# Optimization experiments

Measured on AMD Instinct MI355X. Metric: run time of the kernel, lower is better.

The kernel has to match this reference:

```python
import jax, jax.numpy as jnp
import numpy as np

# Dims: batch B, seq L, embed D, router hidden H, num_blocks NB, top_k K
B, L, D, H, NB, K = 8, 4096, 1024, 64, 16, 2
TEMP = 2.0          # current_temperature buffer (init 2.0), clamp(min=0.1) inert
LN_EPS = 1e-5


def setup_inputs() -> dict:
    key = jax.random.key(0)
    k_x, k_w1, k_w2 = jax.random.split(key, 3)
    return {
        "x": jax.random.normal(k_x, (B, L, D), dtype=jnp.float32),
        "ln_gamma": jnp.ones((D,), dtype=jnp.float32),
        "ln_beta": jnp.zeros((D,), dtype=jnp.float32),
        "W1": jax.random.normal(k_w1, (D, H), dtype=jnp.float32) / np.sqrt(D).astype(np.float32),
        "W2": jax.random.normal(k_w2, (H, NB), dtype=jnp.float32) / np.sqrt(H).astype(np.float32),
    }


def reference(x, ln_gamma, ln_beta, W1, W2):
    # gate: LayerNorm -> Linear(no bias) -> GELU(exact) -> Linear(no bias)
    mu = jnp.mean(x, axis=-1, keepdims=True)
    var = jnp.mean(jnp.square(x - mu), axis=-1, keepdims=True)
    xn = (x - mu) * jax.lax.rsqrt(var + LN_EPS) * ln_gamma + ln_beta
    h = jax.nn.gelu(xn @ W1, approximate=False)          # (B, L, H)
    logits = (h @ W2) / TEMP                              # (B, L, NB)

    probs = jax.nn.softmax(logits, axis=-1)               # (B, L, NB)
    top_probs, indices = jax.lax.top_k(probs, K)          # (B, L, K) each
    weights = top_probs / (jnp.sum(top_probs, axis=-1, keepdims=True) + 1e-8)

    # load-balancing aux loss: f = fraction of assignments per block (detached),
    # P = mean router prob per block
    counts = jnp.zeros((NB,), dtype=probs.dtype).at[indices.reshape(-1)].add(1.0)
    f = jax.lax.stop_gradient(counts) / (B * L * K + 1e-8)
    P = jnp.mean(probs, axis=(0, 1))                      # (NB,)
    aux_loss = NB * jnp.sum(f * P)

    return probs, indices, aux_loss, weights
```

## Files before the change

kernel.cpp:

```cpp
#include <hip/hip_runtime.h>
#include <math.h>

typedef __attribute__((ext_vector_type(8))) short short8;
typedef __attribute__((ext_vector_type(4))) float f32x4;

#define NTOK 32768
#define DDIM 1024
#define HDIM 64
#define NB 16
#define LN_EPS 1e-5f

#define IDX_OFF ((size_t)NTOK * NB)
#define AUX_OFF (IDX_OFF + (size_t)NTOK * 2)
#define WT_OFF  (AUX_OFF + 1)

#define CS_F   64
#define BP_F   4352
#define PART_F 102656

__device__ __forceinline__ short8 as_s8(uint4 u) {
    union { uint4 u; short8 s; } x; x.u = u; return x.s;
}

__device__ __forceinline__ f32x4 ntload4(const float* p) {
    return __builtin_nontemporal_load((const f32x4*)p);
}

__global__ void pack_kernel(const float* __restrict__ W1,
                            const float* __restrict__ gamma,
                            const float* __restrict__ beta,
                            float* __restrict__ ws) {
    __shared__ float sg[4][64];
    __shared__ float sb[4][64];
    const int s = blockIdx.x;
    const int t = threadIdx.x;

    {
        const int j = t & 63, p = t >> 6;
        float ag = 0.f, ab = 0.f;
        for (int kk = 0; kk < 8; ++kk) {
            const int k = s * 32 + p * 8 + kk;
            const float w = W1[k * HDIM + j];
            ag += gamma[k] * w;
            ab += beta[k] * w;
        }
        sg[p][j] = ag;
        sb[p][j] = ab;
    }

    {
        unsigned int* bp = (unsigned int*)(ws + BP_F);
        const int n = t >> 6;
        const int l = t & 63;
        const int q = l >> 4, c = l & 15;
        const int col = n * 16 + c;
        unsigned int uh[8], um[8], ul[8];
#pragma unroll
        for (int j = 0; j < 8; ++j) {
            const int k = s * 32 + q * 8 + j;
            const float w = gamma[k] * W1[k * HDIM + col];
            const unsigned int hb = __float_as_uint(w) & 0xFFFF0000u;
            const float r = w - __uint_as_float(hb);
            const unsigned int mb = __float_as_uint(r) & 0xFFFF0000u;
            const float r2 = r - __uint_as_float(mb);
            const unsigned int lb = __float_as_uint(r2) & 0xFFFF0000u;
            uh[j] = hb >> 16; um[j] = mb >> 16; ul[j] = lb >> 16;
        }
        const int base = ((s * 4 + n) * 64 + l) * 4;
#pragma unroll
        for (int d = 0; d < 4; ++d) {
            bp[base + d]         = uh[2 * d] | (uh[2 * d + 1] << 16);
            bp[32768 + base + d] = um[2 * d] | (um[2 * d + 1] << 16);
            bp[65536 + base + d] = ul[2 * d] | (ul[2 * d + 1] << 16);
        }
    }
    __syncthreads();
    if (t < 64) {
        atomicAdd(&ws[CS_F + t],      sg[0][t] + sg[1][t] + sg[2][t] + sg[3][t]);
        atomicAdd(&ws[CS_F + 64 + t], sb[0][t] + sb[1][t] + sb[2][t] + sb[3][t]);
    }
}

__device__ __forceinline__ void split8(const f32x4 a0, const f32x4 a1,
                                       short8& AH, short8& AM, short8& AL,
                                       float& s1, float& s2) {
    const float v[8] = {a0.x, a0.y, a0.z, a0.w, a1.x, a1.y, a1.z, a1.w};
    unsigned int ph[4], pm[4], pl[4];
#pragma unroll
    for (int d = 0; d < 4; ++d) {
        const float v0 = v[2 * d], v1 = v[2 * d + 1];
        const unsigned int h0 = __float_as_uint(v0) & 0xFFFF0000u;
        const unsigned int h1 = __float_as_uint(v1) & 0xFFFF0000u;
        const float r0 = v0 - __uint_as_float(h0);
        const float r1 = v1 - __uint_as_float(h1);
        const unsigned int m0 = __float_as_uint(r0) & 0xFFFF0000u;
        const unsigned int m1 = __float_as_uint(r1) & 0xFFFF0000u;
        const float q0 = r0 - __uint_as_float(m0);
        const float q1 = r1 - __uint_as_float(m1);
        ph[d] = (h0 >> 16) | h1;
        pm[d] = (m0 >> 16) | m1;
        pl[d] = (__float_as_uint(q0) >> 16) | (__float_as_uint(q1) & 0xFFFF0000u);
        s1 += v0 + v1;
        s2 = fmaf(v0, v0, fmaf(v1, v1, s2));
    }
    AH = as_s8(make_uint4(ph[0], ph[1], ph[2], ph[3]));
    AM = as_s8(make_uint4(pm[0], pm[1], pm[2], pm[3]));
    AL = as_s8(make_uint4(pl[0], pl[1], pl[2], pl[3]));
}

#define MFMA6(ACC, AH, AM, AL, BH, BM, BL)                                        \
    ACC = __builtin_amdgcn_mfma_f32_16x16x32_bf16(AH, as_s8(BH), ACC, 0, 0, 0);   \
    ACC = __builtin_amdgcn_mfma_f32_16x16x32_bf16(AH, as_s8(BM), ACC, 0, 0, 0);   \
    ACC = __builtin_amdgcn_mfma_f32_16x16x32_bf16(AM, as_s8(BH), ACC, 0, 0, 0);   \
    ACC = __builtin_amdgcn_mfma_f32_16x16x32_bf16(AH, as_s8(BL), ACC, 0, 0, 0);   \
    ACC = __builtin_amdgcn_mfma_f32_16x16x32_bf16(AM, as_s8(BM), ACC, 0, 0, 0);   \
    ACC = __builtin_amdgcn_mfma_f32_16x16x32_bf16(AL, as_s8(BH), ACC, 0, 0, 0);

#define STEP(S, CUR, NXT, DOSTAGE)                                               \
    {                                                                            \
        const int off = (((S) + 2) & 31) * 32;                                   \
        const f32x4 p00 = ntload4(xr0 + off), p01 = ntload4(xr0 + off + 4);      \
        const f32x4 p10 = ntload4(xr1 + off), p11 = ntload4(xr1 + off + 4);      \
        uint4 st0, st1, st2;                                                     \
        if (DOSTAGE) {                                                           \
            const unsigned int* sp = bp + ((S) + 1) * 1024 + t * 4;              \
            st0 = *(const uint4*)(sp);                                           \
            st1 = *(const uint4*)(sp + 32768);                                   \
            st2 = *(const uint4*)(sp + 65536);                                   \
        }                                                                        \
        short8 AH0, AM0, AL0, AH1, AM1, AL1;                                     \
        split8(a00, a01, AH0, AM0, AL0, s1a, s2a);                               \
        split8(a10, a11, AH1, AM1, AL1, s1b, s2b);                               \
        _Pragma("unroll")                                                        \
        for (int n = 0; n < 4; ++n) {                                            \
            const uint4 bh = *(const uint4*)((CUR) + n * 256 + lane * 4);        \
            const uint4 bm = *(const uint4*)((CUR) + 1024 + n * 256 + lane * 4); \
            const uint4 bl = *(const uint4*)((CUR) + 2048 + n * 256 + lane * 4); \
            MFMA6(acc0[n], AH0, AM0, AL0, bh, bm, bl);                           \
            MFMA6(acc1[n], AH1, AM1, AL1, bh, bm, bl);                           \
        }                                                                        \
        a00 = b00; a01 = b01; a10 = b10; a11 = b11;                              \
        b00 = p00; b01 = p01; b10 = p10; b11 = p11;                              \
        if (DOSTAGE) {                                                           \
            *(uint4*)((NXT) + t * 4)        = st0;                               \
            *(uint4*)((NXT) + 1024 + t * 4) = st1;                               \
            *(uint4*)((NXT) + 2048 + t * 4) = st2;                               \
        }                                                                        \
        __syncthreads();                                                         \
    }

__global__ __launch_bounds__(256, 2)
void router_main(const float* __restrict__ x,
                 const float* __restrict__ ws_ro,
                 const unsigned int* __restrict__ bp,
                 const float* __restrict__ W2,
                 float* __restrict__ part,
                 float* __restrict__ out) {
    __shared__ __align__(16) float smem[14480];
    float* bstage = smem;
    float* hlds   = smem + 6144;
    float* cntl   = smem + 14464;
    float* w2l    = smem;
    float* llds   = smem + 1024;

    const int t    = threadIdx.x;
    const int wv   = t >> 6;
    const int lane = t & 63;
    const int q = lane >> 4, c = lane & 15;
    const int tok0 = blockIdx.x * 128;
    const int tokw = tok0 + wv * 32;

    if (t < 16) cntl[t] = 0.f;

    float csg[4], csb[4];
#pragma unroll
    for (int n = 0; n < 4; ++n) {
        csg[n] = ws_ro[CS_F + n * 16 + c];
        csb[n] = ws_ro[CS_F + 64 + n * 16 + c];
    }

    const float* xr0 = x + (size_t)(tokw + c) * DDIM + q * 8;
    const float* xr1 = xr0 + (size_t)16 * DDIM;

    {
        uint4 s0 = *(const uint4*)(bp + t * 4);
        uint4 s1 = *(const uint4*)(bp + 32768 + t * 4);
        uint4 s2 = *(const uint4*)(bp + 65536 + t * 4);
        *(uint4*)(bstage + t * 4)        = s0;
        *(uint4*)(bstage + 1024 + t * 4) = s1;
        *(uint4*)(bstage + 2048 + t * 4) = s2;
    }

    f32x4 acc0[4] = {{0.f,0.f,0.f,0.f},{0.f,0.f,0.f,0.f},{0.f,0.f,0.f,0.f},{0.f,0.f,0.f,0.f}};
    f32x4 acc1[4] = {{0.f,0.f,0.f,0.f},{0.f,0.f,0.f,0.f},{0.f,0.f,0.f,0.f},{0.f,0.f,0.f,0.f}};
    float s1a = 0.f, s2a = 0.f, s1b = 0.f, s2b = 0.f;

    f32x4 a00 = ntload4(xr0),      a01 = ntload4(xr0 + 4);
    f32x4 a10 = ntload4(xr1),      a11 = ntload4(xr1 + 4);
    f32x4 b00 = ntload4(xr0 + 32), b01 = ntload4(xr0 + 36);
    f32x4 b10 = ntload4(xr1 + 32), b11 = ntload4(xr1 + 36);

    __syncthreads();

    float* const bufA = bstage;
    float* const bufB = bstage + 3072;
#pragma unroll 1
    for (int s2i = 0; s2i < 16; ++s2i) {
        const int s = s2i * 2;
        STEP(s,     bufA, bufB, 1)
        STEP(s + 1, bufB, bufA, (s2i < 15))
    }

    s1a += __shfl_xor(s1a, 16, 64); s1a += __shfl_xor(s1a, 32, 64);
    s2a += __shfl_xor(s2a, 16, 64); s2a += __shfl_xor(s2a, 32, 64);
    s1b += __shfl_xor(s1b, 16, 64); s1b += __shfl_xor(s1b, 32, 64);
    s2b += __shfl_xor(s2b, 16, 64); s2b += __shfl_xor(s2b, 32, 64);

    *(float4*)(w2l + t * 4) = *(const float4*)(W2 + t * 4);

    {
        float* hw = hlds + wv * 2080;
#pragma unroll
        for (int r = 0; r < 4; ++r) {
            const int tt = q * 4 + r;
            const float S1A = __shfl(s1a, tt, 64), S2A = __shfl(s2a, tt, 64);
            const float S1B = __shfl(s1b, tt, 64), S2B = __shfl(s2b, tt, 64);
            const float muA = S1A * (1.0f / 1024.0f);
            const float rsA = 1.0f / sqrtf(S2A * (1.0f / 1024.0f) - muA * muA + LN_EPS);
            const float muB = S1B * (1.0f / 1024.0f);
            const float rsB = 1.0f / sqrtf(S2B * (1.0f / 1024.0f) - muB * muB + LN_EPS);
#pragma unroll
            for (int n = 0; n < 4; ++n) {
                const float preA = rsA * (acc0[n][r] - muA * csg[n]) + csb[n];
                const float preB = rsB * (acc1[n][r] - muB * csg[n]) + csb[n];
                hw[tt * 65 + n * 16 + c] =
                    0.5f * preA * (1.0f + erff(preA * 0.70710678118654752f));
                hw[(16 + tt) * 65 + n * 16 + c] =
                    0.5f * preB * (1.0f + erff(preB * 0.70710678118654752f));
            }
        }
    }
    __syncthreads();

    {
        const int m2 = t >> 1, o = (t & 1) * 8;
        const float* hrow = hlds + (m2 >> 5) * 2080 + (m2 & 31) * 65;
        f32x4 L0 = {0.f, 0.f, 0.f, 0.f}, L1 = {0.f, 0.f, 0.f, 0.f};
#pragma unroll 8
        for (int j = 0; j < 64; ++j) {
            const float h = hrow[j];
            L0 += *(const f32x4*)(w2l + j * 16 + o) * h;
            L1 += *(const f32x4*)(w2l + j * 16 + o + 4) * h;
        }
        *(f32x4*)(llds + m2 * 16 + o)     = L0 * 0.5f;
        *(f32x4*)(llds + m2 * 16 + o + 4) = L1 * 0.5f;
    }
    __syncthreads();

    if (t < 128) {
        float p[16];
        float mx = -1e30f;
#pragma unroll
        for (int i = 0; i < NB; ++i) { p[i] = llds[t * 16 + i]; mx = fmaxf(mx, p[i]); }
        float ssum = 0.f;
#pragma unroll
        for (int i = 0; i < NB; ++i) { p[i] = expf(p[i] - mx); ssum += p[i]; }
        const float inv = 1.0f / ssum;
#pragma unroll
        for (int i = 0; i < NB; ++i) { p[i] *= inv; llds[t * 16 + i] = p[i]; }

        float* po = out + (size_t)(tok0 + t) * NB;
#pragma unroll
        for (int u = 0; u < 4; ++u) {
            float4 v; v.x = p[u*4]; v.y = p[u*4+1]; v.z = p[u*4+2]; v.w = p[u*4+3];
            *(float4*)(po + u * 4) = v;
        }

        float b0 = -1.f, b1 = -1.f;
        int i0 = 0, i1 = 0;
#pragma unroll
        for (int i = 0; i < NB; ++i) {
            if (p[i] > b0)      { b1 = b0; i1 = i0; b0 = p[i]; i0 = i; }
            else if (p[i] > b1) { b1 = p[i]; i1 = i; }
        }
        const float wsum = b0 + b1 + 1e-8f;
        out[IDX_OFF + (size_t)(tok0 + t) * 2]     = (float)i0;
        out[IDX_OFF + (size_t)(tok0 + t) * 2 + 1] = (float)i1;
        out[WT_OFF + (size_t)(tok0 + t) * 2]      = b0 / wsum;
        out[WT_OFF + (size_t)(tok0 + t) * 2 + 1]  = b1 / wsum;
        atomicAdd(&cntl[i0], 1.0f);
        atomicAdd(&cntl[i1], 1.0f);
    }
    __syncthreads();

    if (t < 16) {
        float ps = 0.f;
        for (int m = 0; m < 128; ++m) ps += llds[m * 16 + t];
        part[(size_t)blockIdx.x * 32 + t]      = cntl[t];
        part[(size_t)blockIdx.x * 32 + 16 + t] = ps;
    }
}

__global__ void aux_kernel(const float* __restrict__ part,
                           float* __restrict__ gacc,
                           float* __restrict__ out) {
    __shared__ float red[8][32];
    __shared__ float flag;
    const int t = threadIdx.x;
    const int b = blockIdx.x;
    const int i = t & 31, rr = t >> 5;
    const int r0 = b * 16 + rr;
    red[rr][i] = part[(size_t)r0 * 32 + i] + part[(size_t)(r0 + 8) * 32 + i];
    __syncthreads();
    if (t < 32) {
        float tot = 0.f;
#pragma unroll
        for (int p = 0; p < 8; ++p) tot += red[p][t];
        atomicAdd(&gacc[t], tot);
    }
    __syncthreads();
    if (t == 0) {
        __threadfence();
        const unsigned int old = atomicAdd((unsigned int*)(gacc + 32), 1u);
        flag = (old == 15u) ? 1.f : 0.f;
    }
    __syncthreads();
    if (flag != 0.f) {
        if (t < 32) red[0][t] = atomicAdd(&gacc[t], 0.0f);
        __syncthreads();
        if (t == 0) {
            float a = 0.f;
            for (int k = 0; k < NB; ++k) {
                const float f = red[0][k] / (65536.0f + 1e-8f);
                const float P = red[0][16 + k] * (1.0f / 32768.0f);
                a += f * P;
            }
            out[AUX_OFF] = 16.0f * a;
        }
    }
}

extern "C" void kernel_launch(void* const* d_in, const int* in_sizes, int n_in,
                              void* d_out, int out_size, void* d_ws, size_t ws_size,
                              hipStream_t stream) {
    const float* x     = (const float*)d_in[0];
    const float* gamma = (const float*)d_in[1];
    const float* beta  = (const float*)d_in[2];
    const float* W1    = (const float*)d_in[3];
    const float* W2    = (const float*)d_in[4];
    float* out = (float*)d_out;
    float* ws  = (float*)d_ws;

    (void)hipMemsetAsync(ws, 0, 192 * sizeof(float), stream);
    pack_kernel<<<32, 256, 0, stream>>>(W1, gamma, beta, ws);
    router_main<<<NTOK / 128, 256, 0, stream>>>(x, ws, (const unsigned int*)(ws + BP_F),
                                                W2, ws + PART_F, out);
    aux_kernel<<<16, 256, 0, stream>>>(ws + PART_F, ws, out);
}
```

Measured before the change: 230.0 us.

## Halve tokens per block and stage W1 slices via global_load_lds

Each wave now handles 16 tokens instead of 32, so blocks cover 64 tokens, the grid doubles and the aux reduction uses 32 blocks. The B-operand staging moves from register loads plus LDS stores to direct global-to-LDS loads issued at the start of each step. Logits storage is padded to a stride of 20 to cut bank conflicts. The intent is lower register and LDS pressure and more resident waves to hide memory latency on x, at the cost of loading the W1 slices twice as often across the whole grid.

```diff
diff --git a/kernel.cpp b/kernel.cpp
--- a/kernel.cpp
+++ b/kernel.cpp
@@ -24,6 +24,12 @@
 
 __device__ __forceinline__ f32x4 ntload4(const float* p) {
     return __builtin_nontemporal_load((const f32x4*)p);
+}
+
+__device__ __forceinline__ void gld16(const unsigned int* g, float* l) {
+    __builtin_amdgcn_global_load_lds(
+        (const __attribute__((address_space(1))) void*)g,
+        (__attribute__((address_space(3))) void*)l, 16, 0, 0);
 }
 
 __global__ void pack_kernel(const float* __restrict__ W1,
@@ -118,34 +124,27 @@
 
 #define STEP(S, CUR, NXT, DOSTAGE)                                               \
     {                                                                            \
+        if (DOSTAGE) {                                                           \
+            _Pragma("unroll")                                                    \
+            for (int i = 0; i < 3; ++i) {                                        \
+                const int idx = wv * 3 + i;                                      \
+                const int term = idx >> 2, nn = idx & 3;                         \
+                gld16(bp + term * 32768 + ((S) + 1) * 1024 + nn * 256 + lane * 4,\
+                      (NXT) + term * 1024 + nn * 256);                           \
+            }                                                                    \
+        }                                                                        \
         const int off = (((S) + 2) & 31) * 32;                                   \
         const f32x4 p00 = ntload4(xr0 + off), p01 = ntload4(xr0 + off + 4);      \
-        const f32x4 p10 = ntload4(xr1 + off), p11 = ntload4(xr1 + off + 4);      \
-        uint4 st0, st1, st2;                                                     \
-        if (DOSTAGE) {                                                           \
-            const unsigned int* sp = bp + ((S) + 1) * 1024 + t * 4;              \
-            st0 = *(const uint4*)(sp);                                           \
-            st1 = *(const uint4*)(sp + 32768);                                   \
-            st2 = *(const uint4*)(sp + 65536);                                   \
-        }                                                                        \
-        short8 AH0, AM0, AL0, AH1, AM1, AL1;                                     \
+        short8 AH0, AM0, AL0;                                                    \
         split8(a00, a01, AH0, AM0, AL0, s1a, s2a);                               \
-        split8(a10, a11, AH1, AM1, AL1, s1b, s2b);                               \
         _Pragma("unroll")                                                        \
         for (int n = 0; n < 4; ++n) {                                            \
             const uint4 bh = *(const uint4*)((CUR) + n * 256 + lane * 4);        \
             const uint4 bm = *(const uint4*)((CUR) + 1024 + n * 256 + lane * 4); \
             const uint4 bl = *(const uint4*)((CUR) + 2048 + n * 256 + lane * 4); \
-            MFMA6(acc0[n], AH0, AM0, AL0, bh, bm, bl);                           \
-            MFMA6(acc1[n], AH1, AM1, AL1, bh, bm, bl);                           \
+            MFMA6(acc[n], AH0, AM0, AL0, bh, bm, bl);                            \
         }                                                                        \
-        a00 = b00; a01 = b01; a10 = b10; a11 = b11;                              \
-        b00 = p00; b01 = p01; b10 = p10; b11 = p11;                              \
-        if (DOSTAGE) {                                                           \
-            *(uint4*)((NXT) + t * 4)        = st0;                               \
-            *(uint4*)((NXT) + 1024 + t * 4) = st1;                               \
-            *(uint4*)((NXT) + 2048 + t * 4) = st2;                               \
-        }                                                                        \
+        a00 = b00; a01 = b01; b00 = p00; b01 = p01;                              \
         __syncthreads();                                                         \
     }
 
@@ -156,10 +155,10 @@
                  const float* __restrict__ W2,
                  float* __restrict__ part,
                  float* __restrict__ out) {
-    __shared__ __align__(16) float smem[14480];
+    __shared__ __align__(16) float smem[10320];
     float* bstage = smem;
     float* hlds   = smem + 6144;
-    float* cntl   = smem + 14464;
+    float* cntl   = smem + 10304;
     float* w2l    = smem;
     float* llds   = smem + 1024;
 
@@ -167,8 +166,8 @@
     const int wv   = t >> 6;
     const int lane = t & 63;
     const int q = lane >> 4, c = lane & 15;
-    const int tok0 = blockIdx.x * 128;
-    const int tokw = tok0 + wv * 32;
+    const int tok0 = blockIdx.x * 64;
+    const int tokw = tok0 + wv * 16;
 
     if (t < 16) cntl[t] = 0.f;
 
@@ -180,30 +179,28 @@
     }
 
     const float* xr0 = x + (size_t)(tokw + c) * DDIM + q * 8;
-    const float* xr1 = xr0 + (size_t)16 * DDIM;
-
-    {
-        uint4 s0 = *(const uint4*)(bp + t * 4);
-        uint4 s1 = *(const uint4*)(bp + 32768 + t * 4);
-        uint4 s2 = *(const uint4*)(bp + 65536 + t * 4);
-        *(uint4*)(bstage + t * 4)        = s0;
-        *(uint4*)(bstage + 1024 + t * 4) = s1;
-        *(uint4*)(bstage + 2048 + t * 4) = s2;
-    }
-
-    f32x4 acc0[4] = {{0.f,0.f,0.f,0.f},{0.f,0.f,0.f,0.f},{0.f,0.f,0.f,0.f},{0.f,0.f,0.f,0.f}};
-    f32x4 acc1[4] = {{0.f,0.f,0.f,0.f},{0.f,0.f,0.f,0.f},{0.f,0.f,0.f,0.f},{0.f,0.f,0.f,0.f}};
-    float s1a = 0.f, s2a = 0.f, s1b = 0.f, s2b = 0.f;
-
-    f32x4 a00 = ntload4(xr0),      a01 = ntload4(xr0 + 4);
-    f32x4 a10 = ntload4(xr1),      a11 = ntload4(xr1 + 4);
-    f32x4 b00 = ntload4(xr0 + 32), b01 = ntload4(xr0 + 36);
-    f32x4 b10 = ntload4(xr1 + 32), b11 = ntload4(xr1 + 36);
-
-    __syncthreads();
 
     float* const bufA = bstage;
     float* const bufB = bstage + 3072;
+
+    {
+#pragma unroll
+        for (int i = 0; i < 3; ++i) {
+            const int idx = wv * 3 + i;
+            const int term = idx >> 2, nn = idx & 3;
+            gld16(bp + term * 32768 + nn * 256 + lane * 4,
+                  bufA + term * 1024 + nn * 256);
+        }
+    }
+
+    f32x4 acc[4] = {{0.f,0.f,0.f,0.f},{0.f,0.f,0.f,0.f},{0.f,0.f,0.f,0.f},{0.f,0.f,0.f,0.f}};
+    float s1a = 0.f, s2a = 0.f;
+
+    f32x4 a00 = ntload4(xr0),      a01 = ntload4(xr0 + 4);
+    f32x4 b00 = ntload4(xr0 + 32), b01 = ntload4(xr0 + 36);
+
+    __syncthreads();
+
 #pragma unroll 1
     for (int s2i = 0; s2i < 16; ++s2i) {
         const int s = s2i * 2;
@@ -213,61 +210,50 @@
 
     s1a += __shfl_xor(s1a, 16, 64); s1a += __shfl_xor(s1a, 32, 64);
     s2a += __shfl_xor(s2a, 16, 64); s2a += __shfl_xor(s2a, 32, 64);
-    s1b += __shfl_xor(s1b, 16, 64); s1b += __shfl_xor(s1b, 32, 64);
-    s2b += __shfl_xor(s2b, 16, 64); s2b += __shfl_xor(s2b, 32, 64);
 
     *(float4*)(w2l + t * 4) = *(const float4*)(W2 + t * 4);
 
     {
-        float* hw = hlds + wv * 2080;
+        float* hw = hlds + wv * 1040;
 #pragma unroll
         for (int r = 0; r < 4; ++r) {
             const int tt = q * 4 + r;
             const float S1A = __shfl(s1a, tt, 64), S2A = __shfl(s2a, tt, 64);
-            const float S1B = __shfl(s1b, tt, 64), S2B = __shfl(s2b, tt, 64);
             const float muA = S1A * (1.0f / 1024.0f);
             const float rsA = 1.0f / sqrtf(S2A * (1.0f / 1024.0f) - muA * muA + LN_EPS);
-            const float muB = S1B * (1.0f / 1024.0f);
-            const float rsB = 1.0f / sqrtf(S2B * (1.0f / 1024.0f) - muB * muB + LN_EPS);
 #pragma unroll
             for (int n = 0; n < 4; ++n) {
-                const float preA = rsA * (acc0[n][r] - muA * csg[n]) + csb[n];
-                const float preB = rsB * (acc1[n][r] - muB * csg[n]) + csb[n];
+                const float preA = rsA * (acc[n][r] - muA * csg[n]) + csb[n];
                 hw[tt * 65 + n * 16 + c] =
                     0.5f * preA * (1.0f + erff(preA * 0.70710678118654752f));
-                hw[(16 + tt) * 65 + n * 16 + c] =
-                    0.5f * preB * (1.0f + erff(preB * 0.70710678118654752f));
             }
         }
     }
     __syncthreads();
 
     {
-        const int m2 = t >> 1, o = (t & 1) * 8;
-        const float* hrow = hlds + (m2 >> 5) * 2080 + (m2 & 31) * 65;
-        f32x4 L0 = {0.f, 0.f, 0.f, 0.f}, L1 = {0.f, 0.f, 0.f, 0.f};
+        const int m2 = t >> 2, o = (t & 3) * 4;
+        const float* hrow = hlds + (m2 >> 4) * 1040 + (m2 & 15) * 65;
+        f32x4 L0 = {0.f, 0.f, 0.f, 0.f};
 #pragma unroll 8
         for (int j = 0; j < 64; ++j) {
-            const float h = hrow[j];
-            L0 += *(const f32x4*)(w2l + j * 16 + o) * h;
-            L1 += *(const f32x4*)(w2l + j * 16 + o + 4) * h;
-        }
-        *(f32x4*)(llds + m2 * 16 + o)     = L0 * 0.5f;
-        *(f32x4*)(llds + m2 * 16 + o + 4) = L1 * 0.5f;
-    }
-    __syncthreads();
-
-    if (t < 128) {
+            L0 += *(const f32x4*)(w2l + j * 16 + o) * hrow[j];
+        }
+        *(f32x4*)(llds + m2 * 20 + o) = L0 * 0.5f;
+    }
+    __syncthreads();
+
+    if (t < 64) {
         float p[16];
         float mx = -1e30f;
 #pragma unroll
-        for (int i = 0; i < NB; ++i) { p[i] = llds[t * 16 + i]; mx = fmaxf(mx, p[i]); }
+        for (int i = 0; i < NB; ++i) { p[i] = llds[t * 20 + i]; mx = fmaxf(mx, p[i]); }
         float ssum = 0.f;
 #pragma unroll
         for (int i = 0; i < NB; ++i) { p[i] = expf(p[i] - mx); ssum += p[i]; }
         const float inv = 1.0f / ssum;
 #pragma unroll
-        for (int i = 0; i < NB; ++i) { p[i] *= inv; llds[t * 16 + i] = p[i]; }
+        for (int i = 0; i < NB; ++i) { p[i] *= inv; llds[t * 20 + i] = p[i]; }
 
         float* po = out + (size_t)(tok0 + t) * NB;
 #pragma unroll
@@ -295,7 +281,7 @@
 
     if (t < 16) {
         float ps = 0.f;
-        for (int m = 0; m < 128; ++m) ps += llds[m * 16 + t];
+        for (int m = 0; m < 64; ++m) ps += llds[m * 20 + t];
         part[(size_t)blockIdx.x * 32 + t]      = cntl[t];
         part[(size_t)blockIdx.x * 32 + 16 + t] = ps;
     }
@@ -322,7 +308,7 @@
     if (t == 0) {
         __threadfence();
         const unsigned int old = atomicAdd((unsigned int*)(gacc + 32), 1u);
-        flag = (old == 15u) ? 1.f : 0.f;
+        flag = (old == 31u) ? 1.f : 0.f;
     }
     __syncthreads();
     if (flag != 0.f) {
@@ -353,7 +339,7 @@
 
     (void)hipMemsetAsync(ws, 0, 192 * sizeof(float), stream);
     pack_kernel<<<32, 256, 0, stream>>>(W1, gamma, beta, ws);
-    router_main<<<NTOK / 128, 256, 0, stream>>>(x, ws, (const unsigned int*)(ws + BP_F),
-                                                W2, ws + PART_F, out);
-    aux_kernel<<<16, 256, 0, stream>>>(ws + PART_F, ws, out);
-}
+    router_main<<<NTOK / 64, 256, 0, stream>>>(x, ws, (const unsigned int*)(ws + BP_F),
+                                               W2, ws + PART_F, out);
+    aux_kernel<<<32, 256, 0, stream>>>(ws + PART_F, ws, out);
+}
```

After: 227.6 us. No clear change (-1.1%).
